# Kernel tuning notes

Measured on AMD Instinct MI355X. Metric: run time of the kernel, lower is better.

Reference implementation:

```python
import jax, jax.numpy as jnp
import numpy as np

B, C, H, L = 4, 1, 1024, 8192
KD, NS = 64, 4  # kernel_dim, num_scales


def _interp_linear(x, out_len):
    """F.interpolate(mode='linear', align_corners=False) along last axis."""
    in_len = x.shape[-1]
    if out_len == in_len:
        return x
    scale = out_len / in_len
    coord = (jnp.arange(out_len, dtype=jnp.float32) + 0.5) / scale - 0.5
    coord = jnp.clip(coord, 0.0, in_len - 1)
    lo = jnp.floor(coord).astype(jnp.int32)
    hi = jnp.minimum(lo + 1, in_len - 1)
    w = coord - lo.astype(jnp.float32)
    return x[..., lo] * (1.0 - w) + x[..., hi] * w


def setup_inputs() -> dict:
    key = jax.random.key(0)
    ks = jax.random.split(key, 8)
    u = jax.random.normal(ks[0], (B, H, L), jnp.float32)
    k0 = jax.random.normal(ks[1], (C, H, KD), jnp.float32)
    k1 = jax.random.normal(ks[2], (C, H, KD), jnp.float32)
    k2 = jax.random.normal(ks[3], (C, H, KD), jnp.float32)
    k3 = jax.random.normal(ks[4], (C, H, KD), jnp.float32)
    D = jax.random.normal(ks[5], (C, H), jnp.float32)
    W = jax.random.normal(ks[6], (H, C * H), jnp.float32) / np.float32(np.sqrt(C * H))
    b = jnp.zeros((H,), jnp.float32)
    return {"u": u, "k0": k0, "k1": k1, "k2": k2, "k3": k3, "D": D, "W": W, "b": b}


def reference(u, k0, k1, k2, k3, D, W, b):
    Lq = u.shape[-1]
    kernels = [k0, k1, k2, k3]
    total = KD * 2 ** (NS - 1)  # 512
    # multi-scale kernel build: interpolate -> right-pad -> scale -> sum
    parts = []
    for i in range(NS):
        ki = _interp_linear(kernels[i], KD * 2 ** i)
        ki = jnp.pad(ki, ((0, 0), (0, 0), (0, total - KD * 2 ** i)))
        parts.append(ki * (2.0 ** (NS - i - 1)))
    k = parts[0] + parts[1] + parts[2] + parts[3]  # (C,H,512)
    # fit to sequence length L
    if k.shape[-1] > Lq:
        k = k[..., :Lq]
    elif k.shape[-1] < Lq:
        k = jnp.pad(k, ((0, 0), (0, 0), (0, Lq - k.shape[-1])))
    # detached kernel norm
    knorm = jax.lax.stop_gradient(
        jnp.linalg.norm(k, axis=-1, keepdims=True))
    k = k / knorm
    # FFT long convolution
    n = 2 * Lq
    k_f = jnp.fft.rfft(k, n=n)              # (C,H,L+1) complex
    u_f = jnp.fft.rfft(u, n=n)              # (B,H,L+1) complex
    y_f = jnp.einsum('bhl,chl->bchl', u_f, k_f)
    y = jnp.fft.irfft(y_f, n=n)[..., :Lq]   # (B,C,H,L)
    # D skip (outer product)
    y = y + jnp.einsum('bhl,ch->bchl', u, D)
    y = y.reshape(y.shape[0], C * H, Lq)    # (B,C*H,L)
    # activation (exact gelu, torch default), dropout=Identity, norm=Identity
    y = jax.nn.gelu(y, approximate=False)
    # output_linear: 1x1 conv (C*H -> H) with bias, Identity post-activation
    y = jnp.einsum('bfl,of->bol', y, W) + b[None, :, None]
    return y
```

## Files before the change

### kernel.cpp

```cpp
#include <hip/hip_runtime.h>
#include <cstdint>
#include <cstddef>

#define HH 1024
#define LL 8192
#define NB 4
#define KD 64
#define KLEN 512

typedef float v4f  __attribute__((ext_vector_type(4)));
typedef float v16f __attribute__((ext_vector_type(16)));
typedef short v8s  __attribute__((ext_vector_type(8)));

__device__ __forceinline__ unsigned short f2bf(float f) {
  union { float f; unsigned int u; } x; x.f = f;
  unsigned int r = x.u + 0x7fffu + ((x.u >> 16) & 1u);
  return (unsigned short)(r >> 16);
}

__global__ __launch_bounds__(512) void build_k_kernel(
    const float* __restrict__ k0, const float* __restrict__ k1,
    const float* __restrict__ k2, const float* __restrict__ k3,
    float* __restrict__ kout) {
  __shared__ float lk[4][KD];
  __shared__ float red[512];
  const int h = blockIdx.x;
  const int t = threadIdx.x;
  if (t < 256) {
    int i = t >> 6, j = t & 63;
    const float* src = (i == 0) ? k0 : (i == 1) ? k1 : (i == 2) ? k2 : k3;
    lk[i][j] = src[h * KD + j];
  }
  __syncthreads();
  float kt = 0.f;
#pragma unroll
  for (int i = 0; i < 4; i++) {
    int len = KD << i;
    if (t < len) {
      float inv = 1.0f / (float)(1 << i);
      float c = ((float)t + 0.5f) * inv - 0.5f;
      c = fminf(fmaxf(c, 0.0f), 63.0f);
      int lo = (int)floorf(c);
      int hi = min(lo + 1, 63);
      float w = c - (float)lo;
      float v = lk[i][lo] * (1.0f - w) + lk[i][hi] * w;
      kt += v * (float)(1 << (3 - i));
    }
  }
  red[t] = kt * kt;
  __syncthreads();
  for (int s = 256; s > 0; s >>= 1) {
    if (t < s) red[t] += red[t + s];
    __syncthreads();
  }
  float norm = sqrtf(red[0]);
  kout[h * KLEN + t] = kt / norm;
}

__global__ void w2bf_kernel(const float* __restrict__ W,
                            unsigned short* __restrict__ Wb, int n) {
  int i = blockIdx.x * blockDim.x + threadIdx.x;
  if (i < n) Wb[i] = f2bf(W[i]);
}

__global__ __launch_bounds__(256) void conv_kernel(
    const float* __restrict__ u, const float* __restrict__ kk,
    const float* __restrict__ D, unsigned short* __restrict__ g) {
  __shared__ __align__(16) unsigned short Apk[34 * 512];
  __shared__ __align__(16) unsigned short su[512 + LL];
  __shared__ __align__(16) float skk[KLEN];

  const int h = blockIdx.x;
  const int tid = threadIdx.x;
  const int w = tid >> 6;
  const int ln = tid & 63;
  const int n = ln & 31;
  const int q = ln >> 5;

  if (tid < 128) *(float4*)(skk + tid * 4) = *(const float4*)(kk + (size_t)h * KLEN + tid * 4);
  __syncthreads();

#pragma unroll 4
  for (int e = 0; e < 68; ++e) {
    int idx = e * 256 + tid;
    int s = idx >> 9;
    int lane = (idx >> 3) & 63;
    int j = idx & 7;
    int m = lane & 31, q2 = lane >> 5;
    int c = ((s & 1) << 4) + (q2 << 3) + j;
    int t = ((s >> 1) << 5) + m - c;
    Apk[idx] = (t >= 0 && t < KLEN) ? f2bf(skk[t]) : (unsigned short)0;
  }

  const float Dh = D[h];
  const int b_base0 = 512 + 32 * (w * 64 + n) + 8 * q;
  const int b_base1 = b_base0 + 1024;

  for (int b = 0; b < NB; ++b) {
    __syncthreads();
    const float* __restrict__ urow = u + ((size_t)b * HH + h) * LL;
    if (tid < 64) {
      uint4 z; z.x = 0; z.y = 0; z.z = 0; z.w = 0;
      *(uint4*)(su + tid * 8) = z;
    }
#pragma unroll
    for (int r = 0; r < 8; ++r) {
      int i = r * 1024 + tid * 4;
      float4 v = *(const float4*)(urow + i);
      uint2 p;
      p.x = (unsigned)f2bf(v.x) | ((unsigned)f2bf(v.y) << 16);
      p.y = (unsigned)f2bf(v.z) | ((unsigned)f2bf(v.w) << 16);
      *(uint2*)(su + 512 + i) = p;
    }
    __syncthreads();

    v16f acc0, acc1;
#pragma unroll
    for (int r = 0; r < 16; ++r) { acc0[r] = 0.f; acc1[r] = 0.f; }

#pragma unroll
    for (int s = 0; s < 34; ++s) {
      const int off = ((s & 1) << 4) - ((s >> 1) << 5);
      v8s af = *(const v8s*)(Apk + (s << 9) + (ln << 3));
      v8s b0 = *(const v8s*)(su + b_base0 + off);
      v8s b1 = *(const v8s*)(su + b_base1 + off);
      acc0 = __builtin_amdgcn_mfma_f32_32x32x16_bf16(af, b0, acc0, 0, 0, 0);
      acc1 = __builtin_amdgcn_mfma_f32_32x32x16_bf16(af, b1, acc1, 0, 0, 0);
    }

    unsigned short* grow = g + ((size_t)b * HH + h) * LL;
#pragma unroll
    for (int t = 0; t < 2; ++t) {
      const int i0 = w * 64 + t * 32;
#pragma unroll
      for (int rg = 0; rg < 4; ++rg) {
        const int l = 32 * (i0 + n) + 8 * rg + 4 * q;
        float4 uu = *(const float4*)(urow + l);
        const float* up = (const float*)&uu;
        unsigned short hb[4];
#pragma unroll
        for (int rr = 0; rr < 4; ++rr) {
          float y = (t ? acc1[rg * 4 + rr] : acc0[rg * 4 + rr]) + Dh * up[rr];
          float ge = 0.5f * y * (1.0f + erff(y * 0.70710678118654752f));
          hb[rr] = f2bf(ge);
        }
        uint2 p;
        p.x = (unsigned)hb[0] | ((unsigned)hb[1] << 16);
        p.y = (unsigned)hb[2] | ((unsigned)hb[3] << 16);
        *(uint2*)(grow + l) = p;
      }
    }
  }
}

__global__ __launch_bounds__(256) void transpose_kernel(
    const unsigned short* __restrict__ g, unsigned short* __restrict__ gt) {
  __shared__ unsigned short s[64][65];
  const int bid = blockIdx.x;
  const int lc = bid & 127;
  const int hc = (bid >> 7) & 15;
  const int b = bid >> 11;
  const int l0 = lc * 64, h0 = hc * 64;
  const int tid = threadIdx.x;
  const int seg = tid & 7, rr = tid >> 3;
#pragma unroll
  for (int p = 0; p < 2; p++) {
    int r = p * 32 + rr;
    uint4 v = *(const uint4*)(g + (size_t)(b * HH + h0 + r) * LL + l0 + seg * 8);
    s[r][seg * 8 + 0] = (unsigned short)(v.x);
    s[r][seg * 8 + 1] = (unsigned short)(v.x >> 16);
    s[r][seg * 8 + 2] = (unsigned short)(v.y);
    s[r][seg * 8 + 3] = (unsigned short)(v.y >> 16);
    s[r][seg * 8 + 4] = (unsigned short)(v.z);
    s[r][seg * 8 + 5] = (unsigned short)(v.z >> 16);
    s[r][seg * 8 + 6] = (unsigned short)(v.w);
    s[r][seg * 8 + 7] = (unsigned short)(v.w >> 16);
  }
  __syncthreads();
#pragma unroll
  for (int p = 0; p < 2; p++) {
    int lr = p * 32 + rr;
    unsigned int a0 = (unsigned)s[seg * 8 + 0][lr] | ((unsigned)s[seg * 8 + 1][lr] << 16);
    unsigned int a1 = (unsigned)s[seg * 8 + 2][lr] | ((unsigned)s[seg * 8 + 3][lr] << 16);
    unsigned int a2 = (unsigned)s[seg * 8 + 4][lr] | ((unsigned)s[seg * 8 + 5][lr] << 16);
    unsigned int a3 = (unsigned)s[seg * 8 + 6][lr] | ((unsigned)s[seg * 8 + 7][lr] << 16);
    uint4 ov; ov.x = a0; ov.y = a1; ov.z = a2; ov.w = a3;
    *(uint4*)(gt + (size_t)(b * LL + l0 + lr) * HH + h0 + seg * 8) = ov;
  }
}

__device__ __forceinline__ void gll16(const void* g, void* l) {
  __builtin_amdgcn_global_load_lds(
      (const __attribute__((address_space(1))) unsigned int*)g,
      (__attribute__((address_space(3))) unsigned int*)l, 16, 0, 0);
}

__global__ __launch_bounds__(256) void gemm_kernel(
    const unsigned short* __restrict__ A,
    const unsigned short* __restrict__ Bt,
    const float* __restrict__ bias, float* __restrict__ out) {
  __shared__ __align__(16) unsigned short sA[128 * 32];
  __shared__ __align__(16) unsigned short sB[128 * 32];
  const int tid = threadIdx.x;
  const int wv = tid >> 6, ln = tid & 63;
  const int bid = blockIdx.x;
  const int mt = bid & 7, nt = bid >> 3;
  const int o0 = mt * 128, n0 = nt * 128;
  const int m16 = ln & 15, q4 = ln >> 4;
  const int wm = wv & 1, wn = wv >> 1;

  v4f acc[4][4];
#pragma unroll
  for (int i = 0; i < 4; i++)
#pragma unroll
    for (int j = 0; j < 4; j++) {
      v4f z = {0.f, 0.f, 0.f, 0.f};
      acc[i][j] = z;
    }

  const unsigned short* gptr[4];
  unsigned short* lptr[4];
#pragma unroll
  for (int qq = 0; qq < 4; qq++) {
    int c = wv * 4 + qq;
    int rr = (c & 7) * 16 + (ln >> 2);
    int cc = (ln & 3) * 8;
    if (c < 8) { gptr[qq] = A  + (size_t)(o0 + rr) * HH + cc; lptr[qq] = sA + c * 512; }
    else       { gptr[qq] = Bt + (size_t)(n0 + rr) * HH + cc; lptr[qq] = sB + (c - 8) * 512; }
  }

  for (int kk = 0; kk < 32; kk++) {
    const int k0 = kk * 32;
#pragma unroll
    for (int qq = 0; qq < 4; qq++) gll16(gptr[qq] + k0, lptr[qq]);
    __syncthreads();
    v8s af[4], bf4[4];
#pragma unroll
    for (int i = 0; i < 4; i++)
      af[i] = *(const v8s*)&sA[(wm * 64 + i * 16 + m16) * 32 + q4 * 8];
#pragma unroll
    for (int i = 0; i < 4; i++)
      bf4[i] = *(const v8s*)&sB[(wn * 64 + i * 16 + m16) * 32 + q4 * 8];
#pragma unroll
    for (int i = 0; i < 4; i++)
#pragma unroll
      for (int j = 0; j < 4; j++)
        acc[i][j] = __builtin_amdgcn_mfma_f32_16x16x32_bf16(af[i], bf4[j], acc[i][j], 0, 0, 0);
    __syncthreads();
  }

#pragma unroll
  for (int i = 0; i < 4; i++) {
    const int ob = o0 + wm * 64 + i * 16 + q4 * 4;
#pragma unroll
    for (int j = 0; j < 4; j++) {
      const int nn = n0 + wn * 64 + j * 16 + m16;
      const int bb = nn >> 13;
      const int l = nn & (LL - 1);
#pragma unroll
      for (int r = 0; r < 4; r++) {
        const int o = ob + r;
        out[(size_t)(bb * HH + o) * LL + l] = acc[i][j][r] + bias[o];
      }
    }
  }
}

extern "C" void kernel_launch(void* const* d_in, const int* in_sizes, int n_in,
                              void* d_out, int out_size, void* d_ws, size_t ws_size,
                              hipStream_t stream) {
  const float* u   = (const float*)d_in[0];
  const float* k0  = (const float*)d_in[1];
  const float* k1  = (const float*)d_in[2];
  const float* k2  = (const float*)d_in[3];
  const float* k3  = (const float*)d_in[4];
  const float* D   = (const float*)d_in[5];
  const float* W   = (const float*)d_in[6];
  const float* bia = (const float*)d_in[7];
  float* out = (float*)d_out;

  char* ws = (char*)d_ws;
  unsigned short* gt = (unsigned short*)ws;
  float* kws         = (float*)(ws + (size_t)67108864);
  unsigned short* Wb = (unsigned short*)(ws + (size_t)69206016);
  unsigned short* g = (unsigned short*)d_out;

  build_k_kernel<<<HH, 512, 0, stream>>>(k0, k1, k2, k3, kws);
  w2bf_kernel<<<(HH * HH + 255) / 256, 256, 0, stream>>>(W, Wb, HH * HH);
  conv_kernel<<<HH, 256, 0, stream>>>(u, kws, D, g);
  transpose_kernel<<<NB * 16 * 128, 256, 0, stream>>>(g, gt);
  gemm_kernel<<<8 * 256, 256, 0, stream>>>(Wb, gt, bia, out);
}
```

Measured before the change: 401.7 us.

## Fuse transpose into GEMM B-tile load with swizzled LDS and register prefetch

Removes the separate transpose kernel. The GEMM now reads the GELU output in its native (b,h,l) layout and packs pairs of k-rows into 32-bit words in a swizzled LDS tile, with a register prefetch of the next k-slab. It also swizzles the block index so blocks sharing the same B tile are grouped, and writes the intermediate to workspace instead of the output buffer. This saves a full read and write of the 64MB bf16 intermediate, at the cost of scalar 4-byte LDS reads per B fragment and more work for the waves that pack B.

```diff
diff --git a/kernel.cpp b/kernel.cpp
--- a/kernel.cpp
+++ b/kernel.cpp
@@ -153,42 +153,6 @@
   }
 }
 
-__global__ __launch_bounds__(256) void transpose_kernel(
-    const unsigned short* __restrict__ g, unsigned short* __restrict__ gt) {
-  __shared__ unsigned short s[64][65];
-  const int bid = blockIdx.x;
-  const int lc = bid & 127;
-  const int hc = (bid >> 7) & 15;
-  const int b = bid >> 11;
-  const int l0 = lc * 64, h0 = hc * 64;
-  const int tid = threadIdx.x;
-  const int seg = tid & 7, rr = tid >> 3;
-#pragma unroll
-  for (int p = 0; p < 2; p++) {
-    int r = p * 32 + rr;
-    uint4 v = *(const uint4*)(g + (size_t)(b * HH + h0 + r) * LL + l0 + seg * 8);
-    s[r][seg * 8 + 0] = (unsigned short)(v.x);
-    s[r][seg * 8 + 1] = (unsigned short)(v.x >> 16);
-    s[r][seg * 8 + 2] = (unsigned short)(v.y);
-    s[r][seg * 8 + 3] = (unsigned short)(v.y >> 16);
-    s[r][seg * 8 + 4] = (unsigned short)(v.z);
-    s[r][seg * 8 + 5] = (unsigned short)(v.z >> 16);
-    s[r][seg * 8 + 6] = (unsigned short)(v.w);
-    s[r][seg * 8 + 7] = (unsigned short)(v.w >> 16);
-  }
-  __syncthreads();
-#pragma unroll
-  for (int p = 0; p < 2; p++) {
-    int lr = p * 32 + rr;
-    unsigned int a0 = (unsigned)s[seg * 8 + 0][lr] | ((unsigned)s[seg * 8 + 1][lr] << 16);
-    unsigned int a1 = (unsigned)s[seg * 8 + 2][lr] | ((unsigned)s[seg * 8 + 3][lr] << 16);
-    unsigned int a2 = (unsigned)s[seg * 8 + 4][lr] | ((unsigned)s[seg * 8 + 5][lr] << 16);
-    unsigned int a3 = (unsigned)s[seg * 8 + 6][lr] | ((unsigned)s[seg * 8 + 7][lr] << 16);
-    uint4 ov; ov.x = a0; ov.y = a1; ov.z = a2; ov.w = a3;
-    *(uint4*)(gt + (size_t)(b * LL + l0 + lr) * HH + h0 + seg * 8) = ov;
-  }
-}
-
 __device__ __forceinline__ void gll16(const void* g, void* l) {
   __builtin_amdgcn_global_load_lds(
       (const __attribute__((address_space(1))) unsigned int*)g,
@@ -197,15 +161,19 @@
 
 __global__ __launch_bounds__(256) void gemm_kernel(
     const unsigned short* __restrict__ A,
-    const unsigned short* __restrict__ Bt,
+    const unsigned short* __restrict__ G,
     const float* __restrict__ bias, float* __restrict__ out) {
   __shared__ __align__(16) unsigned short sA[128 * 32];
-  __shared__ __align__(16) unsigned short sB[128 * 32];
+  __shared__ __align__(16) unsigned int   sB[16 * 128];
   const int tid = threadIdx.x;
   const int wv = tid >> 6, ln = tid & 63;
-  const int bid = blockIdx.x;
-  const int mt = bid & 7, nt = bid >> 3;
-  const int o0 = mt * 128, n0 = nt * 128;
+
+  const int bid0 = blockIdx.x;
+  const int swz = (bid0 & 7) * 256 + (bid0 >> 3);
+  const int mt = swz & 7, nt = swz >> 3;
+  const int o0 = mt * 128;
+  const int bb = nt >> 6;
+  const int l0 = (nt & 63) * 128;
   const int m16 = ln & 15, q4 = ln >> 4;
   const int wm = wv & 1, wn = wv >> 1;
 
@@ -218,29 +186,69 @@
       acc[i][j] = z;
     }
 
-  const unsigned short* gptr[4];
-  unsigned short* lptr[4];
-#pragma unroll
-  for (int qq = 0; qq < 4; qq++) {
-    int c = wv * 4 + qq;
-    int rr = (c & 7) * 16 + (ln >> 2);
-    int cc = (ln & 3) * 8;
-    if (c < 8) { gptr[qq] = A  + (size_t)(o0 + rr) * HH + cc; lptr[qq] = sA + c * 512; }
-    else       { gptr[qq] = Bt + (size_t)(n0 + rr) * HH + cc; lptr[qq] = sB + (c - 8) * 512; }
-  }
+  const unsigned short* gptrA[4];
+  unsigned short* lptrA[4];
+  if (wv < 2) {
+#pragma unroll
+    for (int qq = 0; qq < 4; qq++) {
+      int c = wv * 4 + qq;
+      int rr = c * 16 + (ln >> 2);
+      int cc = (ln & 3) * 8;
+      gptrA[qq] = A + (size_t)(o0 + rr) * HH + cc;
+      lptrA[qq] = sA + c * 512;
+    }
+  }
+
+  const int kp = tid >> 4;
+  const int seg = tid & 15;
+  char* sBb = (char*)sB;
+  const unsigned xw = ((unsigned)(kp & 1) << 4) | ((unsigned)((kp >> 2) & 1) << 6);
+  const unsigned wb0 = (unsigned)(kp * 512 + seg * 32);
+  const unsigned short* gB0 = G + ((size_t)bb * HH + kp * 2) * LL + l0 + seg * 8;
+  const unsigned short* gB1 = gB0 + LL;
+
+  const int nloc = wn * 64 + m16;
+
+  uint4 ra = *(const uint4*)(gB0);
+  uint4 rb = *(const uint4*)(gB1);
 
   for (int kk = 0; kk < 32; kk++) {
-    const int k0 = kk * 32;
-#pragma unroll
-    for (int qq = 0; qq < 4; qq++) gll16(gptr[qq] + k0, lptr[qq]);
-    __syncthreads();
-    v8s af[4], bf4[4];
+    union { uint4 u; unsigned short s[8]; } ua, ub;
+    ua.u = ra; ub.u = rb;
+    unsigned pk[8];
+#pragma unroll
+    for (int i = 0; i < 8; ++i)
+      pk[i] = (unsigned)ua.s[i] | ((unsigned)ub.s[i] << 16);
+    *(uint4*)(sBb + ((wb0)      ^ xw)) = *(const uint4*)&pk[0];
+    *(uint4*)(sBb + ((wb0 + 16) ^ xw)) = *(const uint4*)&pk[4];
+
+    if (wv < 2) {
+#pragma unroll
+      for (int qq = 0; qq < 4; qq++) gll16(gptrA[qq] + kk * 32, lptrA[qq]);
+    }
+    __syncthreads();
+
+    if (kk < 31) {
+      ra = *(const uint4*)(gB0 + (size_t)(kk + 1) * 32 * LL);
+      rb = *(const uint4*)(gB1 + (size_t)(kk + 1) * 32 * LL);
+    }
+
+    v8s af[4];
 #pragma unroll
     for (int i = 0; i < 4; i++)
       af[i] = *(const v8s*)&sA[(wm * 64 + i * 16 + m16) * 32 + q4 * 8];
-#pragma unroll
-    for (int i = 0; i < 4; i++)
-      bf4[i] = *(const v8s*)&sB[(wn * 64 + i * 16 + m16) * 32 + q4 * 8];
+    v8s bf4[4];
+#pragma unroll
+    for (int j = 0; j < 4; j++) {
+      union { v8s v; unsigned w[4]; } u;
+#pragma unroll
+      for (int p = 0; p < 4; p++) {
+        unsigned boff = ((unsigned)((q4 * 4 + p) * 128 + nloc + j * 16) << 2)
+                        ^ ((unsigned)(p & 1) << 4) ^ ((unsigned)(q4 & 1) << 6);
+        u.w[p] = *(const unsigned*)(sBb + boff);
+      }
+      bf4[j] = u.v;
+    }
 #pragma unroll
     for (int i = 0; i < 4; i++)
 #pragma unroll
@@ -254,13 +262,11 @@
     const int ob = o0 + wm * 64 + i * 16 + q4 * 4;
 #pragma unroll
     for (int j = 0; j < 4; j++) {
-      const int nn = n0 + wn * 64 + j * 16 + m16;
-      const int bb = nn >> 13;
-      const int l = nn & (LL - 1);
+      const int l = l0 + wn * 64 + j * 16 + m16;
 #pragma unroll
       for (int r = 0; r < 4; r++) {
         const int o = ob + r;
-        out[(size_t)(bb * HH + o) * LL + l] = acc[i][j][r] + bias[o];
+        out[((size_t)bb * HH + o) * LL + l] = acc[i][j][r] + bias[o];
       }
     }
   }
@@ -280,14 +286,12 @@
   float* out = (float*)d_out;
 
   char* ws = (char*)d_ws;
-  unsigned short* gt = (unsigned short*)ws;
+  unsigned short* g  = (unsigned short*)ws;
   float* kws         = (float*)(ws + (size_t)67108864);
   unsigned short* Wb = (unsigned short*)(ws + (size_t)69206016);
-  unsigned short* g = (unsigned short*)d_out;
 
   build_k_kernel<<<HH, 512, 0, stream>>>(k0, k1, k2, k3, kws);
   w2bf_kernel<<<(HH * HH + 255) / 256, 256, 0, stream>>>(W, Wb, HH * HH);
   conv_kernel<<<HH, 256, 0, stream>>>(u, kws, D, g);
-  transpose_kernel<<<NB * 16 * 128, 256, 0, stream>>>(g, gt);
-  gemm_kernel<<<8 * 256, 256, 0, stream>>>(Wb, gt, bia, out);
-}
+  gemm_kernel<<<8 * 256, 256, 0, stream>>>(Wb, g, bia, out);
+}
```

Result: no change. 399.2 us (-0.6%).
